# Optimization experiments

Hardware: AMD Instinct MI355X
Metric: run time of the kernel (lower is better)

## Reference

```python
import jax, jax.numpy as jnp
import numpy as np

D_MODEL = 512
N_HEAD = 8
D_K = D_MODEL // N_HEAD
B, S = 4, 2048


def setup_inputs() -> dict:
    key = jax.random.key(0)
    ks = jax.random.split(key, 13)
    scale = 1.0 / np.sqrt(D_MODEL)
    inp = {
        "query": jax.random.normal(ks[0], (B, S, D_MODEL), jnp.float32),
        "key": jax.random.normal(ks[1], (B, S, D_MODEL), jnp.float32),
        "value": jax.random.normal(ks[2], (B, S, D_MODEL), jnp.float32),
        "mask": jax.random.randint(ks[3], (B, S, S), 0, 2).astype(bool),
        "Wq": jax.random.normal(ks[4], (D_MODEL, D_MODEL), jnp.float32) * scale,
        "bq": jax.random.normal(ks[5], (D_MODEL,), jnp.float32) * scale,
        "Wk": jax.random.normal(ks[6], (D_MODEL, D_MODEL), jnp.float32) * scale,
        "bk": jax.random.normal(ks[7], (D_MODEL,), jnp.float32) * scale,
        "Wv": jax.random.normal(ks[8], (D_MODEL, D_MODEL), jnp.float32) * scale,
        "bv": jax.random.normal(ks[9], (D_MODEL,), jnp.float32) * scale,
        "Wo": jax.random.normal(ks[10], (D_MODEL, D_MODEL), jnp.float32) * scale,
        "bo": jax.random.normal(ks[11], (D_MODEL,), jnp.float32) * scale,
    }
    return inp


def reference(query, key, value, mask, Wq, bq, Wk, bk, Wv, bv, Wo, bo):
    b = query.shape[0]
    # QKV projections -> [b, h, s, d_k]
    q = (query @ Wq.T + bq).reshape(b, -1, N_HEAD, D_K).transpose(0, 2, 1, 3)
    k = (key @ Wk.T + bk).reshape(b, -1, N_HEAD, D_K).transpose(0, 2, 1, 3)
    v = (value @ Wv.T + bv).reshape(b, -1, N_HEAD, D_K).transpose(0, 2, 1, 3)
    # scaled dot-product scores [b, h, sq, sk]
    scores = jnp.einsum("bhqd,bhkd->bhqk", q, k) / jnp.sqrt(jnp.float32(D_K))
    # masked_fill(mask, -1e4): mask broadcast over heads
    scores = jnp.where(mask[:, None, :, :], jnp.float32(-10000.0), scores)
    attn = jax.nn.softmax(scores, axis=-1)
    x = jnp.einsum("bhqk,bhkd->bhqd", attn, v)
    x = x.transpose(0, 2, 1, 3).reshape(b, -1, N_HEAD * D_K)
    return x @ Wo.T + bo
```

## Files before the change

kernel.cpp:

```cpp
#include <hip/hip_runtime.h>
#include <hip/hip_bf16.h>

#define DMODEL 512
#define NHEAD  8
#define DKH    64
#define SEQ    2048
#define NB     4
#define LOG2E  1.44269504088896f

typedef float f32x4 __attribute__((ext_vector_type(4)));
typedef float f32x16 __attribute__((ext_vector_type(16)));
typedef short bf16x8 __attribute__((ext_vector_type(8)));

__device__ __forceinline__ unsigned short f2bf(float x) {
    unsigned int u = __float_as_uint(x);
    u += 0x7fffu + ((u >> 16) & 1u);
    return (unsigned short)(u >> 16);
}

__device__ __forceinline__ void gload16(const void* g, void* l) {
    __builtin_amdgcn_global_load_lds(
        (const __attribute__((address_space(1))) unsigned int*)g,
        (__attribute__((address_space(3))) unsigned int*)l, 16, 0, 0);
}

__device__ __forceinline__ unsigned int cvtpk(float lo, float hi) {
    unsigned int r;
    asm("v_cvt_pk_bf16_f32 %0, %1, %2" : "=v"(r) : "v"(lo), "v"(hi));
    return r;
}

#define CVT_BLOCKS  6656
#define PACK_BLOCKS 1024
struct PrepArgs {
    const float* src[7]; unsigned short* dst[7];
    const unsigned char* mask; unsigned long long* bits;
};

__global__ __launch_bounds__(256) void prep(PrepArgs a)
{
    const int bx = blockIdx.x;
    if (bx < CVT_BLOCKS) {
        int seg, base;
        if (bx < 6144) { seg = bx >> 11; base = bx & 2047; }
        else           { const int w = bx - 6144; seg = 3 + (w >> 7); base = w & 127; }
        const int i = (base * 256 + threadIdx.x) * 8;
        const float* s = a.src[seg];
        const float4 v0 = *reinterpret_cast<const float4*>(s + i);
        const float4 v1 = *reinterpret_cast<const float4*>(s + i + 4);
        ushort4 h0, h1;
        h0.x = f2bf(v0.x); h0.y = f2bf(v0.y); h0.z = f2bf(v0.z); h0.w = f2bf(v0.w);
        h1.x = f2bf(v1.x); h1.y = f2bf(v1.y); h1.z = f2bf(v1.z); h1.w = f2bf(v1.w);
        *reinterpret_cast<ushort4*>(a.dst[seg] + i)     = h0;
        *reinterpret_cast<ushort4*>(a.dst[seg] + i + 4) = h1;
    } else {
        __shared__ int anyb;
        if (threadIdx.x == 0) anyb = 0;
        __syncthreads();
        const uint4 dv = *reinterpret_cast<const uint4*>(a.mask + threadIdx.x * 16);
        if ((dv.x | dv.y | dv.z | dv.w) & 0xFFFFFF00u) atomicOr(&anyb, 1);
        __syncthreads();
        const int bytemode = anyb;

        const int w = (bx - CVT_BLOCKS) * 256 + threadIdx.x;
        const int b = w >> 16, kt = (w >> 11) & 31, row = w & 2047;
        const size_t eoff = ((size_t)(b * SEQ + row)) * SEQ + kt * 64;
        unsigned long long word = 0;
        if (bytemode) {
            const unsigned char* mp = a.mask + eoff;
            #pragma unroll
            for (int c = 0; c < 4; ++c) {
                const uint4 v = *reinterpret_cast<const uint4*>(mp + c * 16);
                const unsigned int n0 = (v.x | (v.x >> 7) | (v.x >> 14) | (v.x >> 21)) & 0xFu;
                const unsigned int n1 = (v.y | (v.y >> 7) | (v.y >> 14) | (v.y >> 21)) & 0xFu;
                const unsigned int n2 = (v.z | (v.z >> 7) | (v.z >> 14) | (v.z >> 21)) & 0xFu;
                const unsigned int n3 = (v.w | (v.w >> 7) | (v.w >> 14) | (v.w >> 21)) & 0xFu;
                const unsigned int ch = n0 | (n1 << 4) | (n2 << 8) | (n3 << 12);
                word |= (unsigned long long)ch << (16 * c);
            }
        } else {
            const unsigned int* mp = (const unsigned int*)a.mask + eoff;
            #pragma unroll
            for (int c = 0; c < 16; ++c) {
                const uint4 v = *reinterpret_cast<const uint4*>(mp + c * 4);
                const unsigned int nb = (v.x | (v.y << 1) | (v.z << 2) | (v.w << 3)) & 0xFu;
                word |= (unsigned long long)nb << (4 * c);
            }
        }
        a.bits[w] = word;
    }
}

struct GemmSet {
    const unsigned short* A; const unsigned short* W; const float* bias;
    unsigned short* outb; float* outf; float scale; int mode;
};
struct Gemm3 { GemmSet s[3]; };

template<int BM>
__global__ __launch_bounds__(256) void gemm_bf16(Gemm3 G)
{
    constexpr int NJ = (BM == 128) ? 4 : 2;
    __shared__ unsigned short As[BM * 64];
    __shared__ unsigned short Bs[128 * 64];

    const GemmSet gs = G.s[blockIdx.z];
    const int tid = threadIdx.x, lane = tid & 63, wv = tid >> 6;
    const int g = lane >> 4, lr = lane & 15;
    const int bm = blockIdx.x * BM, bn = blockIdx.y * 128;
    const int wm = (BM == 128) ? (wv & 1) * 64 : 0;
    const int wn = (BM == 128) ? (wv >> 1) * 64 : wv * 32;
    const int srow = lane >> 3;
    const int scol = 8 * ((lane & 7) ^ srow);

    f32x4 acc[4][NJ] = {};

    for (int kt = 0; kt < DMODEL; kt += 64) {
        __syncthreads();
        #pragma unroll
        for (int i = 0; i < BM / 32; ++i) {
            const int ch = i * 4 + wv;
            const int row = ch * 8 + srow;
            gload16(&gs.A[(size_t)(bm + row) * DMODEL + kt + scol], &As[ch * 512 + lane * 8]);
        }
        #pragma unroll
        for (int i = 0; i < 4; ++i) {
            const int ch = i * 4 + wv;
            const int row = ch * 8 + srow;
            gload16(&gs.W[(size_t)(bn + row) * DMODEL + kt + scol], &Bs[ch * 512 + lane * 8]);
        }
        __syncthreads();

        #pragma unroll
        for (int kk = 0; kk < 2; ++kk) {
            bf16x8 af[4], bfr[NJ];
            #pragma unroll
            for (int x = 0; x < 4; ++x) {
                const int ra = wm + x * 16 + lr;
                af[x] = *reinterpret_cast<const bf16x8*>(
                    (const char*)As + ((ra * 128 + kk * 64 + g * 16) ^ ((ra & 7) << 4)));
            }
            #pragma unroll
            for (int y = 0; y < NJ; ++y) {
                const int rb = wn + y * 16 + lr;
                bfr[y] = *reinterpret_cast<const bf16x8*>(
                    (const char*)Bs + ((rb * 128 + kk * 64 + g * 16) ^ ((rb & 7) << 4)));
            }
            __builtin_amdgcn_s_setprio(1);
            #pragma unroll
            for (int mi = 0; mi < 4; ++mi)
                #pragma unroll
                for (int nj = 0; nj < NJ; ++nj)
                    acc[mi][nj] = __builtin_amdgcn_mfma_f32_16x16x32_bf16(af[mi], bfr[nj], acc[mi][nj], 0, 0, 0);
            __builtin_amdgcn_s_setprio(0);
        }
    }

    const int mode = gs.mode;
    #pragma unroll
    for (int mi = 0; mi < 4; ++mi) {
        #pragma unroll
        for (int nj = 0; nj < NJ; ++nj) {
            const int col  = bn + wn + nj * 16 + lr;
            const int row0 = bm + wm + mi * 16 + g * 4;
            const float bv = gs.bias[col];
            if (mode == 2) {
                const int bb = row0 >> 11, ss = row0 & (SEQ - 1);
                const int hh = col >> 6,  dd = col & 63;
                ushort4 pk;
                pk.x = f2bf(acc[mi][nj][0] + bv);
                pk.y = f2bf(acc[mi][nj][1] + bv);
                pk.z = f2bf(acc[mi][nj][2] + bv);
                pk.w = f2bf(acc[mi][nj][3] + bv);
                *reinterpret_cast<ushort4*>(&gs.outb[((size_t)((bb * NHEAD + hh) * DKH + dd)) * SEQ + ss]) = pk;
            } else if (mode == 3) {
                #pragma unroll
                for (int r = 0; r < 4; ++r)
                    gs.outf[(size_t)(row0 + r) * DMODEL + col] = acc[mi][nj][r] + bv;
            } else {
                #pragma unroll
                for (int r = 0; r < 4; ++r)
                    gs.outb[(size_t)(row0 + r) * DMODEL + col] = f2bf((acc[mi][nj][r] + bv) * gs.scale);
            }
        }
    }
}

__global__ __launch_bounds__(256) void attn_fwd(
    const unsigned short* __restrict__ Q,
    const unsigned short* __restrict__ K,
    const unsigned short* __restrict__ Vt,
    const unsigned long long* __restrict__ bits,
    unsigned short* __restrict__ X)
{
    __shared__ unsigned short Ks[2][2][64 * 64];
    __shared__ unsigned short Vs[2][2][64 * 64];

    const int tid = threadIdx.x, lane = tid & 63, wv = tid >> 6;
    const int lr32 = lane & 31, hi = lane >> 5;
    const int bid = blockIdx.x;
    const int wg  = (bid & 7) * 64 + (bid >> 3);
    const int qb = wg & 15, h = (wg >> 4) & 7, b = wg >> 7;
    const int q0 = qb * 128, qw = q0 + wv * 32;

    const unsigned short* Kbh = K  + (size_t)b * SEQ * DMODEL + h * DKH;
    const unsigned short* Vbh = Vt + (size_t)(b * NHEAD + h) * DKH * SEQ;
    const unsigned long long* bitsb = bits + (size_t)b * 32 * SEQ + qw + lr32;

    bf16x8 qf[4];
    #pragma unroll
    for (int kd = 0; kd < 4; ++kd)
        qf[kd] = *reinterpret_cast<const bf16x8*>(
            &Q[(size_t)(b * SEQ + qw + lr32) * DMODEL + h * DKH + kd * 16 + hi * 8]);

    const int srow = lane >> 3;
    const int scol = 8 * ((lane & 7) ^ srow);

    auto stage = [&](int buf, int c) {
        #pragma unroll
        for (int i = 0; i < 4; ++i) {
            const int ch   = i * 4 + wv;
            const int half = ch >> 3;
            const int chh  = ch & 7;
            const int row  = chh * 8 + srow;
            const int kt   = c * 128 + half * 64;
            gload16(&Kbh[(size_t)(kt + row) * DMODEL + scol], &Ks[buf][half][chh * 512 + lane * 8]);
            gload16(&Vbh[(size_t)row * SEQ + kt + scol],      &Vs[buf][half][chh * 512 + lane * 8]);
        }
    };

    union { unsigned int u[4]; bf16x8 v; } onesu;
    onesu.u[0] = onesu.u[1] = onesu.u[2] = onesu.u[3] = 0x3F803F80u;
    const bf16x8 ones = onesu.v;

    f32x16 o0 = {}, o1 = {}, o_sum = {};

    stage(0, 0);
    stage(1, 1);

    for (int t = 0; t < 16; ++t) {
        const int cur = t & 1;

        if (t < 15) asm volatile("s_waitcnt vmcnt(8)" ::: "memory");
        else        asm volatile("s_waitcnt vmcnt(0)" ::: "memory");
        __builtin_amdgcn_sched_barrier(0);
        __builtin_amdgcn_s_barrier();

        const unsigned long long mwA = bitsb[(size_t)(2 * t)     * SEQ];
        const unsigned long long mwB = bitsb[(size_t)(2 * t + 1) * SEQ];

        f32x16 sA0 = {}, sA1 = {}, sB0 = {}, sB1 = {};
        __builtin_amdgcn_s_setprio(1);
        #pragma unroll
        for (int kd = 0; kd < 4; ++kd) {
            const int cb = kd * 32 + hi * 16;
            const int r0 = lr32, r1 = 32 + lr32;
            const bf16x8 kfA0 = *reinterpret_cast<const bf16x8*>(
                (const char*)Ks[cur][0] + ((r0 * 128 + cb) ^ ((r0 & 7) << 4)));
            const bf16x8 kfA1 = *reinterpret_cast<const bf16x8*>(
                (const char*)Ks[cur][0] + ((r1 * 128 + cb) ^ ((r1 & 7) << 4)));
            const bf16x8 kfB0 = *reinterpret_cast<const bf16x8*>(
                (const char*)Ks[cur][1] + ((r0 * 128 + cb) ^ ((r0 & 7) << 4)));
            const bf16x8 kfB1 = *reinterpret_cast<const bf16x8*>(
                (const char*)Ks[cur][1] + ((r1 * 128 + cb) ^ ((r1 & 7) << 4)));
            sA0 = __builtin_amdgcn_mfma_f32_32x32x16_bf16(kfA0, qf[kd], sA0, 0, 0, 0);
            sA1 = __builtin_amdgcn_mfma_f32_32x32x16_bf16(kfA1, qf[kd], sA1, 0, 0, 0);
            sB0 = __builtin_amdgcn_mfma_f32_32x32x16_bf16(kfB0, qf[kd], sB0, 0, 0, 0);
            sB1 = __builtin_amdgcn_mfma_f32_32x32x16_bf16(kfB1, qf[kd], sB1, 0, 0, 0);
        }
        __builtin_amdgcn_s_setprio(0);

        auto subtile = [&](const f32x16& s0, const f32x16& s1,
                           unsigned long long mw, int sub) {
            const unsigned long long msh = mw >> (4 * hi);
            const unsigned int mlo = (unsigned int)msh;
            const unsigned int mhi = (unsigned int)(msh >> 32);
            unsigned int pk[8][2];
            #pragma unroll
            for (int kj = 0; kj < 2; ++kj) {
                const unsigned int msel = kj ? mhi : mlo;
                #pragma unroll
                for (int o2 = 0; o2 < 4; ++o2) {
                    float p[4];
                    #pragma unroll
                    for (int r = 0; r < 4; ++r) {
                        const int bitp = o2 * 8 + r;
                        const float mf = (float)(msel & (1u << bitp));
                        const float coef = -1024.f / (float)(1u << bitp);
                        const float sv = kj ? s1[o2 * 4 + r] : s0[o2 * 4 + r];
                        p[r] = exp2f(__builtin_fmaf(mf, coef, sv));
                    }
                    pk[kj * 4 + o2][0] = cvtpk(p[0], p[1]);
                    pk[kj * 4 + o2][1] = cvtpk(p[2], p[3]);
                }
            }
            #pragma unroll
            for (int kk = 0; kk < 4; ++kk) {
                unsigned int a0 = pk[2 * kk][0], b0 = pk[2 * kk + 1][0];
                unsigned int a1 = pk[2 * kk][1], b1 = pk[2 * kk + 1][1];
                asm("v_permlane32_swap_b32 %0, %1" : "+v"(a0), "+v"(b0));
                asm("v_permlane32_swap_b32 %0, %1" : "+v"(a1), "+v"(b1));
                union { unsigned int u[4]; bf16x8 v; } fr;
                fr.u[0] = a0; fr.u[1] = a1; fr.u[2] = b0; fr.u[3] = b1;
                const int cb = kk * 32 + hi * 16;
                const int d0 = lr32, d1 = 32 + lr32;
                const bf16x8 vf0 = *reinterpret_cast<const bf16x8*>(
                    (const char*)Vs[cur][sub] + ((d0 * 128 + cb) ^ ((d0 & 7) << 4)));
                const bf16x8 vf1 = *reinterpret_cast<const bf16x8*>(
                    (const char*)Vs[cur][sub] + ((d1 * 128 + cb) ^ ((d1 & 7) << 4)));
                __builtin_amdgcn_s_setprio(1);
                o0    = __builtin_amdgcn_mfma_f32_32x32x16_bf16(fr.v, vf0, o0, 0, 0, 0);
                o1    = __builtin_amdgcn_mfma_f32_32x32x16_bf16(fr.v, vf1, o1, 0, 0, 0);
                o_sum = __builtin_amdgcn_mfma_f32_32x32x16_bf16(fr.v, ones, o_sum, 0, 0, 0);
                __builtin_amdgcn_s_setprio(0);
            }
        };
        subtile(sA0, sA1, mwA, 0);
        subtile(sB0, sB1, mwB, 1);

        __builtin_amdgcn_s_barrier();
        if (t + 2 <= 15) stage(cur, t + 2);
    }

    #pragma unroll
    for (int r = 0; r < 16; ++r) {
        const int qr = (r & 3) + 8 * (r >> 2) + 4 * hi;
        const float rv = 1.f / o_sum[r];
        const size_t rowoff = (size_t)(b * SEQ + qw + qr) * DMODEL + h * DKH + lr32;
        X[rowoff]      = f2bf(o0[r] * rv);
        X[rowoff + 32] = f2bf(o1[r] * rv);
    }
}

extern "C" void kernel_launch(void* const* d_in, const int* in_sizes, int n_in,
                              void* d_out, int out_size, void* d_ws, size_t ws_size,
                              hipStream_t stream)
{
    const float* query = (const float*)d_in[0];
    const float* key   = (const float*)d_in[1];
    const float* value = (const float*)d_in[2];
    const unsigned char* mask = (const unsigned char*)d_in[3];
    const float* Wq = (const float*)d_in[4];
    const float* bq = (const float*)d_in[5];
    const float* Wk = (const float*)d_in[6];
    const float* bk = (const float*)d_in[7];
    const float* Wv = (const float*)d_in[8];
    const float* bv = (const float*)d_in[9];
    const float* Wo = (const float*)d_in[10];
    const float* bo = (const float*)d_in[11];

    const size_t E = (size_t)(NB * SEQ) * DMODEL;
    const size_t WE = (size_t)DMODEL * DMODEL;
    unsigned short* Qc  = (unsigned short*)d_ws;
    unsigned short* Kc  = Qc + E;
    unsigned short* Vc  = Kc + E;
    unsigned short* Qp  = Vc + E;
    unsigned short* Kp  = Qp + E;
    unsigned short* Vtp = Kp + E;
    unsigned short* Wqb = Vtp + E;
    unsigned short* Wkb = Wqb + WE;
    unsigned short* Wvb = Wkb + WE;
    unsigned short* Wob = Wvb + WE;
    unsigned long long* bits = (unsigned long long*)(Wob + WE);
    unsigned short* Xp = Qc;

    PrepArgs pa;
    pa.src[0] = query; pa.src[1] = key; pa.src[2] = value;
    pa.src[3] = Wq; pa.src[4] = Wk; pa.src[5] = Wv; pa.src[6] = Wo;
    pa.dst[0] = Qc; pa.dst[1] = Kc; pa.dst[2] = Vc;
    pa.dst[3] = Wqb; pa.dst[4] = Wkb; pa.dst[5] = Wvb; pa.dst[6] = Wob;
    pa.mask = mask; pa.bits = bits;
    prep<<<dim3(CVT_BLOCKS + PACK_BLOCKS), 256, 0, stream>>>(pa);

    Gemm3 gq;
    gq.s[0] = { Qc, Wqb, bq, Qp,  nullptr, 0.125f * LOG2E, 0 };
    gq.s[1] = { Kc, Wkb, bk, Kp,  nullptr, 1.0f,   0 };
    gq.s[2] = { Vc, Wvb, bv, Vtp, nullptr, 1.0f,   2 };
    gemm_bf16<128><<<dim3(64, 4, 3), 256, 0, stream>>>(gq);

    attn_fwd<<<dim3(512), 256, 0, stream>>>(Qp, Kp, Vtp, bits, Xp);

    Gemm3 go;
    go.s[0] = { Xp, Wob, bo, nullptr, (float*)d_out, 1.0f, 3 };
    go.s[1] = go.s[0]; go.s[2] = go.s[0];
    gemm_bf16<64><<<dim3(128, 4, 1), 256, 0, stream>>>(go);
}
```

Before: 143.2 us.

## Fuse fp32-to-bf16 activation conversion into QKV projection GEMM loads

The QKV GEMM now reads fp32 query/key/value directly, prefetching the next K-tile into registers and converting to bf16 with v_cvt_pk_bf16_f32 before storing into swizzled LDS. The prep kernel only converts weights and packs the mask, so the separate activation conversion pass and its bf16 workspace round-trip go away. In exchange the A-tile loads go through registers instead of direct global-to-LDS loads, which raises register pressure, and each fp32 A element is read once per N-block.

After: 135.6 us, median of 2. 5.3% less time.

```diff
diff --git a/kernel.cpp b/kernel.cpp
--- a/kernel.cpp
+++ b/kernel.cpp
@@ -30,10 +30,10 @@
     return r;
 }
 
-#define CVT_BLOCKS  6656
+#define CVT_BLOCKS  512
 #define PACK_BLOCKS 1024
 struct PrepArgs {
-    const float* src[7]; unsigned short* dst[7];
+    const float* src[4]; unsigned short* dst[4];
     const unsigned char* mask; unsigned long long* bits;
 };
 
@@ -41,9 +41,7 @@
 {
     const int bx = blockIdx.x;
     if (bx < CVT_BLOCKS) {
-        int seg, base;
-        if (bx < 6144) { seg = bx >> 11; base = bx & 2047; }
-        else           { const int w = bx - 6144; seg = 3 + (w >> 7); base = w & 127; }
+        const int seg = bx >> 7, base = bx & 127;
         const int i = (base * 256 + threadIdx.x) * 8;
         const float* s = a.src[seg];
         const float4 v0 = *reinterpret_cast<const float4*>(s + i);
@@ -92,12 +90,12 @@
 }
 
 struct GemmSet {
-    const unsigned short* A; const unsigned short* W; const float* bias;
+    const void* A; const unsigned short* W; const float* bias;
     unsigned short* outb; float* outf; float scale; int mode;
 };
 struct Gemm3 { GemmSet s[3]; };
 
-template<int BM>
+template<int BM, bool AF32>
 __global__ __launch_bounds__(256) void gemm_bf16(Gemm3 G)
 {
     constexpr int NJ = (BM == 128) ? 4 : 2;
@@ -113,15 +111,44 @@
     const int srow = lane >> 3;
     const int scol = 8 * ((lane & 7) ^ srow);
 
+    const int arow  = tid >> 1;
+    const int ahalf = tid & 1;
+
     f32x4 acc[4][NJ] = {};
-
+    float4 ra[8];
+
+    if constexpr (AF32) {
+        const float* Af = (const float*)gs.A;
+        #pragma unroll
+        for (int j = 0; j < 4; ++j) {
+            const size_t gb = (size_t)(bm + arow) * DMODEL + ahalf * 32 + j * 8;
+            ra[2*j]   = *reinterpret_cast<const float4*>(&Af[gb]);
+            ra[2*j+1] = *reinterpret_cast<const float4*>(&Af[gb + 4]);
+        }
+    }
+
+    #pragma unroll
     for (int kt = 0; kt < DMODEL; kt += 64) {
         __syncthreads();
-        #pragma unroll
-        for (int i = 0; i < BM / 32; ++i) {
-            const int ch = i * 4 + wv;
-            const int row = ch * 8 + srow;
-            gload16(&gs.A[(size_t)(bm + row) * DMODEL + kt + scol], &As[ch * 512 + lane * 8]);
+        if constexpr (AF32) {
+            #pragma unroll
+            for (int j = 0; j < 4; ++j) {
+                unsigned int w0 = cvtpk(ra[2*j].x,   ra[2*j].y);
+                unsigned int w1 = cvtpk(ra[2*j].z,   ra[2*j].w);
+                unsigned int w2 = cvtpk(ra[2*j+1].x, ra[2*j+1].y);
+                unsigned int w3 = cvtpk(ra[2*j+1].z, ra[2*j+1].w);
+                uint4 pkd; pkd.x = w0; pkd.y = w1; pkd.z = w2; pkd.w = w3;
+                const int boff = (arow * 128 + ahalf * 64 + j * 16) ^ ((arow & 7) << 4);
+                *reinterpret_cast<uint4*>((char*)As + boff) = pkd;
+            }
+        } else {
+            #pragma unroll
+            for (int i = 0; i < BM / 32; ++i) {
+                const int ch = i * 4 + wv;
+                const int row = ch * 8 + srow;
+                gload16(&((const unsigned short*)gs.A)[(size_t)(bm + row) * DMODEL + kt + scol],
+                        &As[ch * 512 + lane * 8]);
+            }
         }
         #pragma unroll
         for (int i = 0; i < 4; ++i) {
@@ -129,6 +156,17 @@
             const int row = ch * 8 + srow;
             gload16(&gs.W[(size_t)(bn + row) * DMODEL + kt + scol], &Bs[ch * 512 + lane * 8]);
         }
+        if constexpr (AF32) {
+            if (kt + 64 < DMODEL) {
+                const float* Af = (const float*)gs.A;
+                #pragma unroll
+                for (int j = 0; j < 4; ++j) {
+                    const size_t gb = (size_t)(bm + arow) * DMODEL + kt + 64 + ahalf * 32 + j * 8;
+                    ra[2*j]   = *reinterpret_cast<const float4*>(&Af[gb]);
+                    ra[2*j+1] = *reinterpret_cast<const float4*>(&Af[gb + 4]);
+                }
+            }
+        }
         __syncthreads();
 
         #pragma unroll
@@ -136,9 +174,9 @@
             bf16x8 af[4], bfr[NJ];
             #pragma unroll
             for (int x = 0; x < 4; ++x) {
-                const int ra = wm + x * 16 + lr;
+                const int ra_ = wm + x * 16 + lr;
                 af[x] = *reinterpret_cast<const bf16x8*>(
-                    (const char*)As + ((ra * 128 + kk * 64 + g * 16) ^ ((ra & 7) << 4)));
+                    (const char*)As + ((ra_ * 128 + kk * 64 + g * 16) ^ ((ra_ & 7) << 4)));
             }
             #pragma unroll
             for (int y = 0; y < NJ; ++y) {
@@ -351,10 +389,8 @@
 
     const size_t E = (size_t)(NB * SEQ) * DMODEL;
     const size_t WE = (size_t)DMODEL * DMODEL;
-    unsigned short* Qc  = (unsigned short*)d_ws;
-    unsigned short* Kc  = Qc + E;
-    unsigned short* Vc  = Kc + E;
-    unsigned short* Qp  = Vc + E;
+    unsigned short* Xp  = (unsigned short*)d_ws;
+    unsigned short* Qp  = Xp + E;
     unsigned short* Kp  = Qp + E;
     unsigned short* Vtp = Kp + E;
     unsigned short* Wqb = Vtp + E;
@@ -362,26 +398,23 @@
     unsigned short* Wvb = Wkb + WE;
     unsigned short* Wob = Wvb + WE;
     unsigned long long* bits = (unsigned long long*)(Wob + WE);
-    unsigned short* Xp = Qc;
 
     PrepArgs pa;
-    pa.src[0] = query; pa.src[1] = key; pa.src[2] = value;
-    pa.src[3] = Wq; pa.src[4] = Wk; pa.src[5] = Wv; pa.src[6] = Wo;
-    pa.dst[0] = Qc; pa.dst[1] = Kc; pa.dst[2] = Vc;
-    pa.dst[3] = Wqb; pa.dst[4] = Wkb; pa.dst[5] = Wvb; pa.dst[6] = Wob;
+    pa.src[0] = Wq; pa.src[1] = Wk; pa.src[2] = Wv; pa.src[3] = Wo;
+    pa.dst[0] = Wqb; pa.dst[1] = Wkb; pa.dst[2] = Wvb; pa.dst[3] = Wob;
     pa.mask = mask; pa.bits = bits;
     prep<<<dim3(CVT_BLOCKS + PACK_BLOCKS), 256, 0, stream>>>(pa);
 
     Gemm3 gq;
-    gq.s[0] = { Qc, Wqb, bq, Qp,  nullptr, 0.125f * LOG2E, 0 };
-    gq.s[1] = { Kc, Wkb, bk, Kp,  nullptr, 1.0f,   0 };
-    gq.s[2] = { Vc, Wvb, bv, Vtp, nullptr, 1.0f,   2 };
-    gemm_bf16<128><<<dim3(64, 4, 3), 256, 0, stream>>>(gq);
+    gq.s[0] = { query, Wqb, bq, Qp,  nullptr, 0.125f * LOG2E, 0 };
+    gq.s[1] = { key,   Wkb, bk, Kp,  nullptr, 1.0f,   0 };
+    gq.s[2] = { value, Wvb, bv, Vtp, nullptr, 1.0f,   2 };
+    gemm_bf16<128, true><<<dim3(64, 4, 3), 256, 0, stream>>>(gq);
 
     attn_fwd<<<dim3(512), 256, 0, stream>>>(Qp, Kp, Vtp, bits, Xp);
 
     Gemm3 go;
     go.s[0] = { Xp, Wob, bo, nullptr, (float*)d_out, 1.0f, 3 };
     go.s[1] = go.s[0]; go.s[2] = go.s[0];
-    gemm_bf16<64><<<dim3(128, 4, 1), 256, 0, stream>>>(go);
-}
+    gemm_bf16<64, false><<<dim3(128, 4, 1), 256, 0, stream>>>(go);
+}
```
